# Kernel tuning notes

Measured on AMD Instinct MI355X. Metric: run time of the kernel, lower is better.

## Reference

```python
import jax, jax.numpy as jnp
import numpy as np

N = 25000
E = 400000
RAW = 64
REP = 64
HID = 128
HEADS = 2
OUT = 2
NEG_SLOPE = 0.2


def setup_inputs() -> dict:
    key = jax.random.key(0)
    ks = jax.random.split(key, 16)
    d_in1 = RAW + REP
    d_h = HID * HEADS
    inp = {
        'x': jax.random.normal(ks[0], (N, RAW), jnp.float32),
        'rep': jax.random.normal(ks[1], (N, REP), jnp.float32),
        'src': jax.random.randint(ks[2], (E,), 0, N, jnp.int32),
        'dst': jax.random.randint(ks[3], (E,), 0, N, jnp.int32),
        # GATConv 1 params
        'W1': jax.random.normal(ks[4], (d_in1, d_h), jnp.float32) * (1.0 / np.sqrt(d_in1)),
        'al1': jax.random.normal(ks[5], (HEADS, HID), jnp.float32) * 0.1,
        'ar1': jax.random.normal(ks[6], (HEADS, HID), jnp.float32) * 0.1,
        'b1': jnp.zeros((HEADS, HID), jnp.float32),
        # GATConv 2 params
        'W2': jax.random.normal(ks[7], (d_h, d_h), jnp.float32) * (1.0 / np.sqrt(d_h)),
        'al2': jax.random.normal(ks[8], (HEADS, HID), jnp.float32) * 0.1,
        'ar2': jax.random.normal(ks[9], (HEADS, HID), jnp.float32) * 0.1,
        'b2': jnp.zeros((HEADS, HID), jnp.float32),
        # final edge classifier
        'fcW': jax.random.normal(ks[10], (d_h * 2, OUT), jnp.float32) * (1.0 / np.sqrt(d_h * 2)),
        'fcb': jnp.zeros((OUT,), jnp.float32),
    }
    return inp


def _gat_conv(feat, W, a_l, a_r, bias, src, dst):
    """DGL-style GATConv: proj -> edge LeakyReLU score -> per-dst softmax -> scatter-sum."""
    n = feat.shape[0]
    h = (feat @ W).reshape(n, HEADS, HID)            # [N,H,D]
    el = jnp.einsum('nhd,hd->nh', h, a_l)            # [N,H]
    er = jnp.einsum('nhd,hd->nh', h, a_r)            # [N,H]
    e = jax.nn.leaky_relu(el[src] + er[dst], NEG_SLOPE)  # [E,H]
    # numerically stable segment softmax over incoming edges of each dst node
    m = jax.ops.segment_max(e, dst, num_segments=n)      # [N,H]
    m = jnp.where(jnp.isfinite(m), m, 0.0)
    ex = jnp.exp(e - m[dst])                             # [E,H]
    s = jax.ops.segment_sum(ex, dst, num_segments=n)     # [N,H]
    alpha = ex / s[dst]                                  # [E,H]
    out = jax.ops.segment_sum(alpha[:, :, None] * h[src], dst, num_segments=n)  # [N,H,D]
    return out + bias[None, :, :]


def reference(x, rep, src, dst, W1, al1, ar1, b1, W2, al2, ar2, b2, fcW, fcb):
    feat = jnp.concatenate([x, rep], axis=-1)                       # [N, RAW+REP]
    h = _gat_conv(feat, W1, al1, ar1, b1, src, dst)                 # [N,H,D]
    h = jax.nn.relu(h.reshape(N, HEADS * HID))                      # [N, H*D]
    h = _gat_conv(h, W2, al2, ar2, b2, src, dst)                    # [N,H,D]
    h = jax.nn.relu(h.reshape(N, HEADS * HID))                      # [N, H*D]
    edge_feat = jnp.concatenate([h[src], h[dst]], axis=1)           # [E, 2*H*D]
    return edge_feat @ fcW + fcb                                    # [E, OUT]
```

## Files before the change

### kernel.cpp

```cpp
#include <hip/hip_runtime.h>
#include <hip/hip_bf16.h>

#define HEADS 2
#define HIDD  128
#define DH    256
#define NEG   0.2f
#define CAP   128

typedef _Float16 half4 __attribute__((ext_vector_type(4)));
typedef float    f32x4 __attribute__((ext_vector_type(4)));


__global__ __launch_bounds__(256) void k_prep(const float* __restrict__ x,
                                              const float* __restrict__ rep,
                                              const float* __restrict__ W1,
                                              const float* __restrict__ W2,
                                              const int* __restrict__ dst,
                                              _Float16* __restrict__ feat16,
                                              _Float16* __restrict__ W1T,
                                              _Float16* __restrict__ W2T,
                                              int* __restrict__ deg,
                                              int N, int E) {
    int gid = blockIdx.x * 256 + threadIdx.x;
    int featQuads = N * 32;
    if (gid < featQuads) {
        int n = gid >> 5, d = (gid & 31) * 4;
        const float* s = (d < 64) ? (x + (size_t)n * 64 + d) : (rep + (size_t)n * 64 + (d - 64));
        float4 v = *reinterpret_cast<const float4*>(s);
        half4 o = { (_Float16)v.x, (_Float16)v.y, (_Float16)v.z, (_Float16)v.w };
        *reinterpret_cast<half4*>(feat16 + (size_t)n * 128 + d) = o;
        return;
    }
    gid -= featQuads;
    if (gid < 256 * 128) {
        int n = gid >> 7, k = gid & 127;
        W1T[n * 128 + k] = (_Float16)W1[(size_t)k * 256 + n];
        return;
    }
    gid -= 256 * 128;
    if (gid < 256 * 256) {
        int n = gid >> 8, k = gid & 255;
        W2T[n * 256 + k] = (_Float16)W2[(size_t)k * 256 + n];
        return;
    }
    gid -= 256 * 256;
    if (gid < E) atomicAdd(&deg[dst[gid]], 1);
}


__global__ __launch_bounds__(1024) void k_scan(const int* __restrict__ deg,
                                               int* __restrict__ row_ptr,
                                               int* __restrict__ cursor, int n) {
    __shared__ int lds[1024];
    int tid = threadIdx.x;
    int base = tid * 32;
    int v[32];
#pragma unroll
    for (int k = 0; k < 8; ++k) {
        int4 q = *reinterpret_cast<const int4*>(deg + base + k * 4);
        v[k * 4 + 0] = q.x; v[k * 4 + 1] = q.y; v[k * 4 + 2] = q.z; v[k * 4 + 3] = q.w;
    }
    int local[32];
    int sum = 0;
#pragma unroll
    for (int k = 0; k < 32; ++k) { local[k] = sum; sum += v[k]; }
    lds[tid] = sum;
    __syncthreads();
    for (int off = 1; off < 1024; off <<= 1) {
        int t = (tid >= off) ? lds[tid - off] : 0;
        __syncthreads();
        lds[tid] += t;
        __syncthreads();
    }
    int thread_off = lds[tid] - sum;
#pragma unroll
    for (int k = 0; k < 32; ++k) {
        int i = base + k;
        if (i < n) {
            int rp = thread_off + local[k];
            row_ptr[i] = rp;
            cursor[i]  = rp;
        }
    }
    if (tid == 1023) row_ptr[n] = lds[1023];
}

__global__ void k_fill(const int* __restrict__ src, const int* __restrict__ dst,
                       int* __restrict__ cursor, int* __restrict__ csr_src, int E) {
    int e = blockIdx.x * blockDim.x + threadIdx.x;
    if (e < E) {
        int pos = atomicAdd(&cursor[dst[e]], 1);
        csr_src[pos] = src[e];
    }
}


#define GBM 64
#define GBN 128
#define GBK 64

template<int K>
__global__ __launch_bounds__(256) void k_gemm16(const _Float16* __restrict__ A,
                                                const _Float16* __restrict__ BT,
                                                _Float16* __restrict__ C16,
                                                const float* __restrict__ alp,
                                                const float* __restrict__ arp,
                                                float* __restrict__ el,
                                                float* __restrict__ er, int M) {
    __shared__ _Float16 As[2][GBM * GBK];
    __shared__ _Float16 Bs[2][GBN * GBK];

    int tid = threadIdx.x;
    int lane = tid & 63;
    int wave = tid >> 6;
    int row0 = blockIdx.x * GBM;
    int col0 = blockIdx.y * GBN;
    int wrow = (wave & 1) * 32;
    int wcol = (wave >> 1) * 64;

    uint4 ra[2], rb[4];
    const int am = tid >> 3;
    const int ak8 = (tid & 7) * 8;

    auto stage_load = [&](int s) {
        const _Float16* ap = A + (size_t)(row0 + am) * K + s * GBK + ak8;
        ra[0] = *reinterpret_cast<const uint4*>(ap);
        ra[1] = *reinterpret_cast<const uint4*>(ap + (size_t)32 * K);
        const _Float16* bp = BT + (size_t)(col0 + am) * K + s * GBK + ak8;
#pragma unroll
        for (int it = 0; it < 4; ++it)
            rb[it] = *reinterpret_cast<const uint4*>(bp + (size_t)(it * 32) * K);
    };
    auto stage_write = [&](int buf) {
        char* ab = (char*)As[buf];
        char* bb = (char*)Bs[buf];
#pragma unroll
        for (int it = 0; it < 2; ++it) {
            int m = am + it * 32;
            int byte = (m * 128 + ak8 * 2) ^ ((m & 7) << 4);
            *reinterpret_cast<uint4*>(ab + byte) = ra[it];
        }
#pragma unroll
        for (int it = 0; it < 4; ++it) {
            int n = am + it * 32;
            int byte = (n * 128 + ak8 * 2) ^ ((n & 7) << 4);
            *reinterpret_cast<uint4*>(bb + byte) = rb[it];
        }
    };

    f32x4 acc[2][4];
#pragma unroll
    for (int i = 0; i < 2; ++i)
#pragma unroll
        for (int j = 0; j < 4; ++j) acc[i][j] = (f32x4){0.f, 0.f, 0.f, 0.f};

    stage_load(0);
    stage_write(0);
    __syncthreads();

    const int S = K / GBK;
    for (int s = 0; s < S; ++s) {
        if (s + 1 < S) stage_load(s + 1);
        const char* ab = (const char*)As[s & 1];
        const char* bb = (const char*)Bs[s & 1];
#pragma unroll
        for (int kk = 0; kk < GBK / 16; ++kk) {
            half4 af[2], bf[4];
#pragma unroll
            for (int i = 0; i < 2; ++i) {
                int m = wrow + i * 16 + (lane & 15);
                int byte = (m * 128 + kk * 32 + (lane >> 4) * 8) ^ ((m & 7) << 4);
                af[i] = *reinterpret_cast<const half4*>(ab + byte);
            }
#pragma unroll
            for (int j = 0; j < 4; ++j) {
                int n = wcol + j * 16 + (lane & 15);
                int byte = (n * 128 + kk * 32 + (lane >> 4) * 8) ^ ((n & 7) << 4);
                bf[j] = *reinterpret_cast<const half4*>(bb + byte);
            }
#pragma unroll
            for (int i = 0; i < 2; ++i)
#pragma unroll
                for (int j = 0; j < 4; ++j)
                    acc[i][j] = __builtin_amdgcn_mfma_f32_16x16x16f16(af[i], bf[j], acc[i][j], 0, 0, 0);
        }
        if (s + 1 < S) stage_write((s + 1) & 1);
        __syncthreads();
    }

    char* Cs = (char*)As;
    {
        int r4 = (lane >> 4) * 4, cl = lane & 15;
#pragma unroll
        for (int i = 0; i < 2; ++i)
#pragma unroll
            for (int j = 0; j < 4; ++j) {
                int col = wcol + j * 16 + cl;
#pragma unroll
                for (int r = 0; r < 4; ++r) {
                    int row = wrow + i * 16 + r4 + r;
                    int byte = (row * 256 + col * 2) ^ ((row & 7) << 4);
                    *reinterpret_cast<_Float16*>(Cs + byte) = (_Float16)acc[i][j][r];
                }
            }
    }
    __syncthreads();

#pragma unroll
    for (int it = 0; it < 4; ++it) {
        int lin = tid + it * 256;
        int row = lin >> 4, chunk = lin & 15;
        int gr = row0 + row;
        if (gr < M) {
            int byte = (row * 256 + chunk * 16) ^ ((row & 7) << 4);
            *reinterpret_cast<uint4*>(C16 + (size_t)gr * DH + col0 + chunk * 8) =
                *reinterpret_cast<const uint4*>(Cs + byte);
        }
    }

    {
        int r = lane >> 2, q = lane & 3;
        int row = wave * 16 + r;
        const float* alg = alp + col0;
        const float* arg = arp + col0;
        float els = 0.f, ers = 0.f;
#pragma unroll
        for (int kk = 0; kk < 4; ++kk) {
            int c0 = q * 32 + kk * 8;
            int byte = (row * 256 + c0 * 2) ^ ((row & 7) << 4);
            uint4 u = *reinterpret_cast<const uint4*>(Cs + byte);
            const _Float16* hv = (const _Float16*)&u;
#pragma unroll
            for (int t = 0; t < 8; ++t) {
                float hvv = (float)hv[t];
                els = fmaf(hvv, alg[c0 + t], els);
                ers = fmaf(hvv, arg[c0 + t], ers);
            }
        }
        els += __shfl_xor(els, 1); els += __shfl_xor(els, 2);
        ers += __shfl_xor(ers, 1); ers += __shfl_xor(ers, 2);
        int gr = row0 + row;
        if (q == 0 && gr < M) {
            el[gr * 2 + blockIdx.y] = els;
            er[gr * 2 + blockIdx.y] = ers;
        }
    }
}


template<bool FINAL>
__global__ __launch_bounds__(256) void k_agg(const _Float16* __restrict__ h,
                                             const float2* __restrict__ el2,
                                             const float2* __restrict__ er2,
                                             const int* __restrict__ row_ptr,
                                             const int* __restrict__ csr_src,
                                             const float* __restrict__ bias,
                                             _Float16* __restrict__ g,
                                             const float* __restrict__ fcW,
                                             float* __restrict__ p, int N) {
    __shared__ int    s_idx[4][CAP];
    __shared__ float2 s_a[4][CAP];

    int w = threadIdx.x >> 6, lane = threadIdx.x & 63;
    int node = blockIdx.x * 4 + w;
    if (node >= N) return;
    int beg = row_ptr[node];
    int deg = row_ptr[node + 1] - beg;
    float2 er = er2[node];
    bool lo = lane < 32;

    float m0 = -__builtin_inff(), m1 = -__builtin_inff();
    for (int i = lane; i < deg; i += 64) {
        int s = csr_src[beg + i];
        float2 el = el2[s];
        float sc0 = el.x + er.x; sc0 = sc0 > 0.f ? sc0 : NEG * sc0;
        float sc1 = el.y + er.y; sc1 = sc1 > 0.f ? sc1 : NEG * sc1;
        if (i < CAP) { s_idx[w][i] = s; s_a[w][i] = make_float2(sc0, sc1); }
        m0 = fmaxf(m0, sc0);
        m1 = fmaxf(m1, sc1);
    }
#pragma unroll
    for (int off = 32; off; off >>= 1) {
        m0 = fmaxf(m0, __shfl_xor(m0, off));
        m1 = fmaxf(m1, __shfl_xor(m1, off));
    }

    float sum0 = 0.f, sum1 = 0.f;
    for (int i = lane; i < deg; i += 64) {
        float2 sc;
        if (i < CAP) sc = s_a[w][i];
        else {
            int s = csr_src[beg + i];
            float2 el = el2[s];
            sc.x = el.x + er.x; sc.x = sc.x > 0.f ? sc.x : NEG * sc.x;
            sc.y = el.y + er.y; sc.y = sc.y > 0.f ? sc.y : NEG * sc.y;
        }
        float e0 = __expf(sc.x - m0);
        float e1 = __expf(sc.y - m1);
        if (i < CAP) s_a[w][i] = make_float2(e0, e1);
        sum0 += e0;
        sum1 += e1;
    }
#pragma unroll
    for (int off = 32; off; off >>= 1) {
        sum0 += __shfl_xor(sum0, off);
        sum1 += __shfl_xor(sum1, off);
    }
    float S   = lo ? sum0 : sum1;
    float inv = S > 0.f ? 1.f / S : 0.f;
    float mh  = lo ? m0 : m1;
    float erh = lo ? er.x : er.y;

    const _Float16* hp = h + lane * 4;
    float4 acc = make_float4(0.f, 0.f, 0.f, 0.f);

#define FETCH(I, S_, A_)                                                    \
    do {                                                                     \
        int _i = (I);                                                        \
        if (_i < CAP) {                                                      \
            S_ = s_idx[w][_i];                                               \
            float2 _a2 = s_a[w][_i];                                         \
            A_ = lo ? _a2.x : _a2.y;                                         \
        } else {                                                             \
            S_ = csr_src[beg + _i];                                          \
            float2 _el = el2[S_];                                            \
            float _sc = (lo ? _el.x : _el.y) + erh;                          \
            _sc = _sc > 0.f ? _sc : NEG * _sc;                               \
            A_ = __expf(_sc - mh);                                           \
        }                                                                    \
    } while (0)

#define ACCUM(V, A_)                                                         \
    do {                                                                     \
        const _Float16* _hv = reinterpret_cast<const _Float16*>(&(V));       \
        acc.x = fmaf(A_, (float)_hv[0], acc.x);                              \
        acc.y = fmaf(A_, (float)_hv[1], acc.y);                              \
        acc.z = fmaf(A_, (float)_hv[2], acc.z);                              \
        acc.w = fmaf(A_, (float)_hv[3], acc.w);                              \
    } while (0)

    int i = 0;
    for (; i + 8 <= deg; i += 8) {
        int ss[8];
        float aa[8];
#pragma unroll
        for (int u = 0; u < 8; ++u) FETCH(i + u, ss[u], aa[u]);
        uint2 vv[8];
#pragma unroll
        for (int u = 0; u < 8; ++u)
            vv[u] = *reinterpret_cast<const uint2*>(hp + (size_t)ss[u] * DH);
#pragma unroll
        for (int u = 0; u < 8; ++u) ACCUM(vv[u], aa[u]);
    }
    for (; i + 4 <= deg; i += 4) {
        int ss[4];
        float aa[4];
#pragma unroll
        for (int u = 0; u < 4; ++u) FETCH(i + u, ss[u], aa[u]);
        uint2 vv[4];
#pragma unroll
        for (int u = 0; u < 4; ++u)
            vv[u] = *reinterpret_cast<const uint2*>(hp + (size_t)ss[u] * DH);
#pragma unroll
        for (int u = 0; u < 4; ++u) ACCUM(vv[u], aa[u]);
    }
    for (; i < deg; ++i) {
        int s;
        float a;
        FETCH(i, s, a);
        uint2 v = *reinterpret_cast<const uint2*>(hp + (size_t)s * DH);
        ACCUM(v, a);
    }
#undef FETCH
#undef ACCUM

    float4 b = *reinterpret_cast<const float4*>(bias + lane * 4);
    float o0 = fmaxf(fmaf(acc.x, inv, b.x), 0.f);
    float o1 = fmaxf(fmaf(acc.y, inv, b.y), 0.f);
    float o2 = fmaxf(fmaf(acc.z, inv, b.z), 0.f);
    float o3 = fmaxf(fmaf(acc.w, inv, b.w), 0.f);

    if (!FINAL) {
        half4 o = { (_Float16)o0, (_Float16)o1, (_Float16)o2, (_Float16)o3 };
        *reinterpret_cast<half4*>(g + (size_t)node * DH + lane * 4) = o;
    } else {
        int d = lane * 4;
        float a0 = 0.f, a1 = 0.f, a2 = 0.f, a3 = 0.f;
        float ov[4] = {o0, o1, o2, o3};
#pragma unroll
        for (int t = 0; t < 4; ++t) {
            float2 wt = *reinterpret_cast<const float2*>(&fcW[(d + t) * 2]);
            float2 wb = *reinterpret_cast<const float2*>(&fcW[(DH + d + t) * 2]);
            a0 = fmaf(ov[t], wt.x, a0);
            a1 = fmaf(ov[t], wt.y, a1);
            a2 = fmaf(ov[t], wb.x, a2);
            a3 = fmaf(ov[t], wb.y, a3);
        }
#pragma unroll
        for (int off = 32; off; off >>= 1) {
            a0 += __shfl_xor(a0, off);
            a1 += __shfl_xor(a1, off);
            a2 += __shfl_xor(a2, off);
            a3 += __shfl_xor(a3, off);
        }
        if (lane == 0)
            *reinterpret_cast<float4*>(&p[(size_t)node * 4]) = make_float4(a0, a1, a2, a3);
    }
}


__global__ void k_edgeout(const float* __restrict__ p,
                          const int* __restrict__ src,
                          const int* __restrict__ dst,
                          const float* __restrict__ fcb,
                          float* __restrict__ out, int E) {
    int e = blockIdx.x * blockDim.x + threadIdx.x;
    if (e >= E) return;
    int s = src[e], d = dst[e];
    float2 ps = *reinterpret_cast<const float2*>(&p[(size_t)s * 4]);
    float2 pd = *reinterpret_cast<const float2*>(&p[(size_t)d * 4 + 2]);
    float2 o;
    o.x = ps.x + pd.x + fcb[0];
    o.y = ps.y + pd.y + fcb[1];
    *reinterpret_cast<float2*>(&out[(size_t)e * 2]) = o;
}


extern "C" void kernel_launch(void* const* d_in, const int* in_sizes, int n_in,
                              void* d_out, int out_size, void* d_ws, size_t ws_size,
                              hipStream_t stream) {
    const float* x   = (const float*)d_in[0];
    const float* rep = (const float*)d_in[1];
    const int*   src = (const int*)d_in[2];
    const int*   dst = (const int*)d_in[3];
    const float* W1  = (const float*)d_in[4];
    const float* al1 = (const float*)d_in[5];
    const float* ar1 = (const float*)d_in[6];
    const float* b1  = (const float*)d_in[7];
    const float* W2  = (const float*)d_in[8];
    const float* al2 = (const float*)d_in[9];
    const float* ar2 = (const float*)d_in[10];
    const float* b2  = (const float*)d_in[11];
    const float* fcW = (const float*)d_in[12];
    const float* fcb = (const float*)d_in[13];
    float* out = (float*)d_out;

    int N = in_sizes[0] / 64;
    int E = in_sizes[2];

    char* ws = (char*)d_ws;
    size_t off = 0;
    auto alloc = [&](size_t bytes) -> void* {
        void* ptr = ws + off;
        off = (off + bytes + 255) & ~(size_t)255;
        return ptr;
    };
    int*       deg     = (int*)alloc((size_t)32768 * 4);
    int*       row_ptr = (int*)alloc((size_t)(N + 1) * 4);
    int*       cursor  = (int*)alloc((size_t)N * 4);
    int*       csr_src = (int*)alloc((size_t)E * 4);
    _Float16*  feat16  = (_Float16*)alloc((size_t)N * 128 * 2);
    _Float16*  W1T     = (_Float16*)alloc((size_t)256 * 128 * 2);
    _Float16*  W2T     = (_Float16*)alloc((size_t)256 * 256 * 2);
    _Float16*  h16     = (_Float16*)alloc((size_t)N * DH * 2);
    _Float16*  g16     = (_Float16*)alloc((size_t)N * DH * 2);
    float*     el      = (float*)alloc((size_t)N * 2 * 4);
    float*     er      = (float*)alloc((size_t)N * 2 * 4);
    float*     p       = (float*)alloc((size_t)N * 4 * 4);
    (void)alloc(65536);

    hipMemsetAsync(deg, 0, (size_t)32768 * 4, stream);

    int eb = (E + 255) / 256;
    int nb4 = (N + 3) / 4;
    int prep_blocks = (N * 32 + 256 * 128 + 256 * 256 + E + 255) / 256;

    k_prep<<<prep_blocks, 256, 0, stream>>>(x, rep, W1, W2, dst, feat16, W1T, W2T, deg, N, E);
    k_scan<<<1, 1024, 0, stream>>>(deg, row_ptr, cursor, N);
    k_fill<<<eb, 256, 0, stream>>>(src, dst, cursor, csr_src, E);

    dim3 ggrid((N + GBM - 1) / GBM, DH / GBN);
    k_gemm16<128><<<ggrid, 256, 0, stream>>>(feat16, W1T, h16, al1, ar1, el, er, N);
    k_agg<false><<<nb4, 256, 0, stream>>>(h16, (const float2*)el, (const float2*)er,
                                          row_ptr, csr_src, b1, g16, nullptr, nullptr, N);
    k_gemm16<256><<<ggrid, 256, 0, stream>>>(g16, W2T, h16, al2, ar2, el, er, N);
    k_agg<true><<<nb4, 256, 0, stream>>>(h16, (const float2*)el, (const float2*)er,
                                         row_ptr, csr_src, b2, nullptr, fcW, p, N);
    k_edgeout<<<eb, 256, 0, stream>>>(p, src, dst, fcb, out, E);
}
```

Measured before the change: 298.3 us.

## Precompute edge softmax weights per edge with atomic sums, drop per-node max pass

Edge attention exponentials are now computed in edge-parallel kernels: the CSR fill is moved after the first GEMM and also writes packed (src, exp0, exp1, dst) records plus atomically accumulated per-destination sums, and a second pass recomputes them for layer 2. The aggregation kernel drops its max and sum passes and just loads packed records into LDS. This removes the per-node max subtraction, so exp without stabilization can overflow for large scores, and float atomics make the sums nondeterministic. The CSR grows from 4 to 16 bytes per edge.

```diff
diff --git a/kernel.cpp b/kernel.cpp
--- a/kernel.cpp
+++ b/kernel.cpp
@@ -9,6 +9,8 @@
 
 typedef _Float16 half4 __attribute__((ext_vector_type(4)));
 typedef float    f32x4 __attribute__((ext_vector_type(4)));
+
+__device__ __forceinline__ float leaky(float x) { return x > 0.f ? x : NEG * x; }
 
 
 __global__ __launch_bounds__(256) void k_prep(const float* __restrict__ x,
@@ -85,13 +87,46 @@
     if (tid == 1023) row_ptr[n] = lds[1023];
 }
 
-__global__ void k_fill(const int* __restrict__ src, const int* __restrict__ dst,
-                       int* __restrict__ cursor, int* __restrict__ csr_src, int E) {
+
+__global__ void k_fill_alpha(const int* __restrict__ src, const int* __restrict__ dst,
+                             int* __restrict__ cursor,
+                             const float2* __restrict__ el2, const float2* __restrict__ er2,
+                             int4* __restrict__ csr16, float* __restrict__ Sarr, int E) {
     int e = blockIdx.x * blockDim.x + threadIdx.x;
-    if (e < E) {
-        int pos = atomicAdd(&cursor[dst[e]], 1);
-        csr_src[pos] = src[e];
-    }
+    if (e >= E) return;
+    int s = src[e], d = dst[e];
+    int pos = atomicAdd(&cursor[d], 1);
+    float2 el = el2[s];
+    float2 er = er2[d];
+    float e0 = __expf(leaky(el.x + er.x));
+    float e1 = __expf(leaky(el.y + er.y));
+    int4 pack;
+    pack.x = s;
+    pack.y = __float_as_int(e0);
+    pack.z = __float_as_int(e1);
+    pack.w = d;
+    csr16[pos] = pack;
+    atomicAdd(&Sarr[d * 2 + 0], e0);
+    atomicAdd(&Sarr[d * 2 + 1], e1);
+}
+
+
+__global__ void k_alpha2(int4* __restrict__ csr16,
+                         const float2* __restrict__ el2, const float2* __restrict__ er2,
+                         float* __restrict__ Sarr, int E) {
+    int i = blockIdx.x * blockDim.x + threadIdx.x;
+    if (i >= E) return;
+    int4 pack = csr16[i];
+    int s = pack.x, d = pack.w;
+    float2 el = el2[s];
+    float2 er = er2[d];
+    float e0 = __expf(leaky(el.x + er.x));
+    float e1 = __expf(leaky(el.y + er.y));
+    pack.y = __float_as_int(e0);
+    pack.z = __float_as_int(e1);
+    csr16[i] = pack;
+    atomicAdd(&Sarr[d * 2 + 0], e0);
+    atomicAdd(&Sarr[d * 2 + 1], e1);
 }
 
 
@@ -250,84 +285,38 @@
 
 template<bool FINAL>
 __global__ __launch_bounds__(256) void k_agg(const _Float16* __restrict__ h,
-                                             const float2* __restrict__ el2,
-                                             const float2* __restrict__ er2,
+                                             const int4* __restrict__ csr16,
+                                             const float* __restrict__ Sarr,
                                              const int* __restrict__ row_ptr,
-                                             const int* __restrict__ csr_src,
                                              const float* __restrict__ bias,
                                              _Float16* __restrict__ g,
                                              const float* __restrict__ fcW,
                                              float* __restrict__ p, int N) {
-    __shared__ int    s_idx[4][CAP];
-    __shared__ float2 s_a[4][CAP];
+    __shared__ int4 s_pack[4][CAP];
 
     int w = threadIdx.x >> 6, lane = threadIdx.x & 63;
     int node = blockIdx.x * 4 + w;
     if (node >= N) return;
     int beg = row_ptr[node];
     int deg = row_ptr[node + 1] - beg;
-    float2 er = er2[node];
     bool lo = lane < 32;
 
-    float m0 = -__builtin_inff(), m1 = -__builtin_inff();
-    for (int i = lane; i < deg; i += 64) {
-        int s = csr_src[beg + i];
-        float2 el = el2[s];
-        float sc0 = el.x + er.x; sc0 = sc0 > 0.f ? sc0 : NEG * sc0;
-        float sc1 = el.y + er.y; sc1 = sc1 > 0.f ? sc1 : NEG * sc1;
-        if (i < CAP) { s_idx[w][i] = s; s_a[w][i] = make_float2(sc0, sc1); }
-        m0 = fmaxf(m0, sc0);
-        m1 = fmaxf(m1, sc1);
-    }
-#pragma unroll
-    for (int off = 32; off; off >>= 1) {
-        m0 = fmaxf(m0, __shfl_xor(m0, off));
-        m1 = fmaxf(m1, __shfl_xor(m1, off));
-    }
-
-    float sum0 = 0.f, sum1 = 0.f;
-    for (int i = lane; i < deg; i += 64) {
-        float2 sc;
-        if (i < CAP) sc = s_a[w][i];
-        else {
-            int s = csr_src[beg + i];
-            float2 el = el2[s];
-            sc.x = el.x + er.x; sc.x = sc.x > 0.f ? sc.x : NEG * sc.x;
-            sc.y = el.y + er.y; sc.y = sc.y > 0.f ? sc.y : NEG * sc.y;
-        }
-        float e0 = __expf(sc.x - m0);
-        float e1 = __expf(sc.y - m1);
-        if (i < CAP) s_a[w][i] = make_float2(e0, e1);
-        sum0 += e0;
-        sum1 += e1;
-    }
-#pragma unroll
-    for (int off = 32; off; off >>= 1) {
-        sum0 += __shfl_xor(sum0, off);
-        sum1 += __shfl_xor(sum1, off);
-    }
-    float S   = lo ? sum0 : sum1;
+    int cap = deg < CAP ? deg : CAP;
+    for (int i = lane; i < cap; i += 64)
+        s_pack[w][i] = csr16[beg + i];
+
+    float S = Sarr[node * 2 + (lo ? 0 : 1)];
     float inv = S > 0.f ? 1.f / S : 0.f;
-    float mh  = lo ? m0 : m1;
-    float erh = lo ? er.x : er.y;
 
     const _Float16* hp = h + lane * 4;
     float4 acc = make_float4(0.f, 0.f, 0.f, 0.f);
 
-#define FETCH(I, S_, A_)                                                    \
+#define FETCH(I, S_, A_)                                                     \
     do {                                                                     \
         int _i = (I);                                                        \
-        if (_i < CAP) {                                                      \
-            S_ = s_idx[w][_i];                                               \
-            float2 _a2 = s_a[w][_i];                                         \
-            A_ = lo ? _a2.x : _a2.y;                                         \
-        } else {                                                             \
-            S_ = csr_src[beg + _i];                                          \
-            float2 _el = el2[S_];                                            \
-            float _sc = (lo ? _el.x : _el.y) + erh;                          \
-            _sc = _sc > 0.f ? _sc : NEG * _sc;                               \
-            A_ = __expf(_sc - mh);                                           \
-        }                                                                    \
+        int4 _p = (_i < CAP) ? s_pack[w][_i] : csr16[beg + _i];              \
+        S_ = _p.x;                                                           \
+        A_ = lo ? __int_as_float(_p.y) : __int_as_float(_p.z);               \
     } while (0)
 
 #define ACCUM(V, A_)                                                         \
@@ -456,9 +445,12 @@
         return ptr;
     };
     int*       deg     = (int*)alloc((size_t)32768 * 4);
+    float*     S1      = (float*)alloc((size_t)N * 2 * 4);
+    float*     S2      = (float*)alloc((size_t)N * 2 * 4);
+    size_t     zbytes  = off;
     int*       row_ptr = (int*)alloc((size_t)(N + 1) * 4);
     int*       cursor  = (int*)alloc((size_t)N * 4);
-    int*       csr_src = (int*)alloc((size_t)E * 4);
+    int4*      csr16   = (int4*)alloc((size_t)E * 16);
     _Float16*  feat16  = (_Float16*)alloc((size_t)N * 128 * 2);
     _Float16*  W1T     = (_Float16*)alloc((size_t)256 * 128 * 2);
     _Float16*  W2T     = (_Float16*)alloc((size_t)256 * 256 * 2);
@@ -469,7 +461,7 @@
     float*     p       = (float*)alloc((size_t)N * 4 * 4);
     (void)alloc(65536);
 
-    hipMemsetAsync(deg, 0, (size_t)32768 * 4, stream);
+    hipMemsetAsync(deg, 0, zbytes, stream);
 
     int eb = (E + 255) / 256;
     int nb4 = (N + 3) / 4;
@@ -477,14 +469,14 @@
 
     k_prep<<<prep_blocks, 256, 0, stream>>>(x, rep, W1, W2, dst, feat16, W1T, W2T, deg, N, E);
     k_scan<<<1, 1024, 0, stream>>>(deg, row_ptr, cursor, N);
-    k_fill<<<eb, 256, 0, stream>>>(src, dst, cursor, csr_src, E);
 
     dim3 ggrid((N + GBM - 1) / GBM, DH / GBN);
     k_gemm16<128><<<ggrid, 256, 0, stream>>>(feat16, W1T, h16, al1, ar1, el, er, N);
-    k_agg<false><<<nb4, 256, 0, stream>>>(h16, (const float2*)el, (const float2*)er,
-                                          row_ptr, csr_src, b1, g16, nullptr, nullptr, N);
+    k_fill_alpha<<<eb, 256, 0, stream>>>(src, dst, cursor, (const float2*)el, (const float2*)er,
+                                         csr16, S1, E);
+    k_agg<false><<<nb4, 256, 0, stream>>>(h16, csr16, S1, row_ptr, b1, g16, nullptr, nullptr, N);
     k_gemm16<256><<<ggrid, 256, 0, stream>>>(g16, W2T, h16, al2, ar2, el, er, N);
-    k_agg<true><<<nb4, 256, 0, stream>>>(h16, (const float2*)el, (const float2*)er,
-                                         row_ptr, csr_src, b2, nullptr, fcW, p, N);
+    k_alpha2<<<eb, 256, 0, stream>>>(csr16, (const float2*)el, (const float2*)er, S2, E);
+    k_agg<true><<<nb4, 256, 0, stream>>>(h16, csr16, S2, row_ptr, b2, nullptr, fcW, p, N);
     k_edgeout<<<eb, 256, 0, stream>>>(p, src, dst, fcb, out, E);
 }
```

After: 393.9 us. +32.0%, slower.
